# Performance work log

Measured on AMD Instinct MI355X. Metric: run time of the kernel, lower is better.

Reference implementation:

```python
import jax, jax.numpy as jnp
import numpy as np

N = 33554432  # number of flattened prediction/target points (~128 MB fp32 each)


def setup_inputs() -> dict:
    key = jax.random.key(0)
    k1, k2 = jax.random.split(key)
    predicted = jax.random.uniform(k1, (N,), dtype=jnp.float32)
    target = jax.random.uniform(k2, (N,), dtype=jnp.float32)
    weights = jnp.array([1.0, 2.0, 4.0, 8.0, 16.0], dtype=jnp.float32)
    edge = jnp.array([0.0, 0.1, 0.25, 0.5, 0.75, 1.0], dtype=jnp.float32)
    return {"predicted": predicted, "target": target, "weights": weights, "edge": edge}


def reference(predicted, target, weights, edge):
    # Original loops over bins: elements with edge[i] < t <= edge[i+1] get weight[i];
    # elements outside (edge[0], edge[-1]] are DROPPED (weight 0).
    nbins = weights.shape[0]
    # digitize(..., right=True): returns i s.t. edge[i-1] < t <= edge[i]; shift to bin index
    bin_idx = jnp.digitize(target, edge, right=True) - 1  # [N] int
    valid = (bin_idx >= 0) & (bin_idx < nbins)
    w = jnp.where(valid, weights[jnp.clip(bin_idx, 0, nbins - 1)], 0.0)
    loss = jnp.sum(w * (predicted - target) ** 2) / jnp.sum(weights)
    return loss
```

## Files before the change

### kernel.cpp

```cpp
#include <hip/hip_runtime.h>


#define NSLOTS 2048

__global__ void wmse_zero_ws(float* __restrict__ ws) {
    ws[blockIdx.x * blockDim.x + threadIdx.x] = 0.0f;
}

__device__ __forceinline__ float wmse_elem(float p, float t,
                                           float e0, float e1, float e2,
                                           float e3, float e4, float e5,
                                           float w0, float w1, float w2,
                                           float w3, float w4) {
    float w = 0.0f;
    w = (t > e0 && t <= e1) ? w0 : w;
    w = (t > e1 && t <= e2) ? w1 : w;
    w = (t > e2 && t <= e3) ? w2 : w;
    w = (t > e3 && t <= e4) ? w3 : w;
    w = (t > e4 && t <= e5) ? w4 : w;
    float d = p - t;
    return w * d * d;
}

__global__ __launch_bounds__(256) void WeightedMSELoss_60335700574782_kernel(
    const float* __restrict__ pred, const float* __restrict__ targ,
    const float* __restrict__ edge, const float* __restrict__ weights,
    float* __restrict__ partial, long long n4) {
    const float e0 = edge[0], e1 = edge[1], e2 = edge[2];
    const float e3 = edge[3], e4 = edge[4], e5 = edge[5];
    const float w0 = weights[0], w1 = weights[1], w2 = weights[2];
    const float w3 = weights[3], w4 = weights[4];

    const long long i = (long long)blockIdx.x * blockDim.x + threadIdx.x;
    const float4* __restrict__ p4 = (const float4*)pred;
    const float4* __restrict__ t4 = (const float4*)targ;

    float acc = 0.0f;
    if (i < n4) {
        float4 p = p4[i];
        float4 t = t4[i];
        acc  = wmse_elem(p.x, t.x, e0, e1, e2, e3, e4, e5, w0, w1, w2, w3, w4);
        acc += wmse_elem(p.y, t.y, e0, e1, e2, e3, e4, e5, w0, w1, w2, w3, w4);
        acc += wmse_elem(p.z, t.z, e0, e1, e2, e3, e4, e5, w0, w1, w2, w3, w4);
        acc += wmse_elem(p.w, t.w, e0, e1, e2, e3, e4, e5, w0, w1, w2, w3, w4);
    }

    #pragma unroll
    for (int off = 32; off > 0; off >>= 1)
        acc += __shfl_down(acc, off, 64);

    __shared__ float smem[4];
    const int lane = threadIdx.x & 63;
    const int wid = threadIdx.x >> 6;
    if (lane == 0) smem[wid] = acc;
    __syncthreads();
    if (threadIdx.x == 0) {
        float bsum = smem[0] + smem[1] + smem[2] + smem[3];
        atomicAdd(&partial[blockIdx.x & (NSLOTS - 1)], bsum);
    }
}

__global__ __launch_bounds__(256) void wmse_finish_kernel(
    const float* __restrict__ partial,
    const float* __restrict__ pred, const float* __restrict__ targ,
    const float* __restrict__ edge, const float* __restrict__ weights,
    float* __restrict__ out, long long n) {
    const float e0 = edge[0], e1 = edge[1], e2 = edge[2];
    const float e3 = edge[3], e4 = edge[4], e5 = edge[5];
    const float w0 = weights[0], w1 = weights[1], w2 = weights[2];
    const float w3 = weights[3], w4 = weights[4];
    const float inv_wsum = 1.0f / (w0 + w1 + w2 + w3 + w4);

    float acc = 0.0f;
    for (int i = threadIdx.x; i < NSLOTS; i += blockDim.x)
        acc += partial[i];

    const long long n4 = n >> 2;
    for (long long j = (n4 << 2) + threadIdx.x; j < n; j += blockDim.x)
        acc += wmse_elem(pred[j], targ[j], e0, e1, e2, e3, e4, e5, w0, w1, w2, w3, w4);

    #pragma unroll
    for (int off = 32; off > 0; off >>= 1)
        acc += __shfl_down(acc, off, 64);

    __shared__ float smem[4];
    const int lane = threadIdx.x & 63;
    const int wid = threadIdx.x >> 6;
    if (lane == 0) smem[wid] = acc;
    __syncthreads();
    if (threadIdx.x == 0)
        out[0] = (smem[0] + smem[1] + smem[2] + smem[3]) * inv_wsum;
}

extern "C" void kernel_launch(void* const* d_in, const int* in_sizes, int n_in,
                              void* d_out, int out_size, void* d_ws, size_t ws_size,
                              hipStream_t stream) {
    const float* pred    = (const float*)d_in[0];
    const float* targ    = (const float*)d_in[1];
    const float* weights = (const float*)d_in[2];
    const float* edge    = (const float*)d_in[3];
    float* out = (float*)d_out;
    float* partial = (float*)d_ws;
    const long long n = (long long)in_sizes[0];
    const long long n4 = n >> 2;

    wmse_zero_ws<<<NSLOTS / 256, 256, 0, stream>>>(partial);

    const int block = 256;
    const int grid = (int)((n4 + block - 1) / block);
    WeightedMSELoss_60335700574782_kernel<<<grid, block, 0, stream>>>(
        pred, targ, edge, weights, partial, n4);

    wmse_finish_kernel<<<1, block, 0, stream>>>(
        partial, pred, targ, edge, weights, out, n);
}
```

Measured before the change: 272.8 us.

## Process eight float4s per thread and write per-block partials without atomics

Each thread now loads eight float4 pairs up front and reduces them with four independent accumulators, so each block covers 2048 float4s and the grid is eight times smaller. Each block writes its sum to its own slot in the workspace, which removes the workspace-zeroing kernel and the atomic adds. The finish kernel now reduces a variable number of partials (4096 here) and handles the leftover tail. More loads in flight per thread give more memory-level parallelism, at the cost of higher register use and a serial finish loop that is twice as long.

```diff
diff --git a/kernel.cpp b/kernel.cpp
--- a/kernel.cpp
+++ b/kernel.cpp
@@ -1,11 +1,5 @@
 #include <hip/hip_runtime.h>
 
-
-#define NSLOTS 2048
-
-__global__ void wmse_zero_ws(float* __restrict__ ws) {
-    ws[blockIdx.x * blockDim.x + threadIdx.x] = 0.0f;
-}
 
 __device__ __forceinline__ float wmse_elem(float p, float t,
                                            float e0, float e1, float e2,
@@ -22,28 +16,49 @@
     return w * d * d;
 }
 
+#define WMSE4(p, t) (                                                          \
+    wmse_elem((p).x, (t).x, e0, e1, e2, e3, e4, e5, w0, w1, w2, w3, w4) +      \
+    wmse_elem((p).y, (t).y, e0, e1, e2, e3, e4, e5, w0, w1, w2, w3, w4) +      \
+    wmse_elem((p).z, (t).z, e0, e1, e2, e3, e4, e5, w0, w1, w2, w3, w4) +      \
+    wmse_elem((p).w, (t).w, e0, e1, e2, e3, e4, e5, w0, w1, w2, w3, w4))
+
+#define PER_BLOCK_F4 2048LL
+
 __global__ __launch_bounds__(256) void WeightedMSELoss_60335700574782_kernel(
     const float* __restrict__ pred, const float* __restrict__ targ,
     const float* __restrict__ edge, const float* __restrict__ weights,
-    float* __restrict__ partial, long long n4) {
+    float* __restrict__ partial) {
     const float e0 = edge[0], e1 = edge[1], e2 = edge[2];
     const float e3 = edge[3], e4 = edge[4], e5 = edge[5];
     const float w0 = weights[0], w1 = weights[1], w2 = weights[2];
     const float w3 = weights[3], w4 = weights[4];
 
-    const long long i = (long long)blockIdx.x * blockDim.x + threadIdx.x;
     const float4* __restrict__ p4 = (const float4*)pred;
     const float4* __restrict__ t4 = (const float4*)targ;
+    const long long base = (long long)blockIdx.x * PER_BLOCK_F4 + threadIdx.x;
 
-    float acc = 0.0f;
-    if (i < n4) {
-        float4 p = p4[i];
-        float4 t = t4[i];
-        acc  = wmse_elem(p.x, t.x, e0, e1, e2, e3, e4, e5, w0, w1, w2, w3, w4);
-        acc += wmse_elem(p.y, t.y, e0, e1, e2, e3, e4, e5, w0, w1, w2, w3, w4);
-        acc += wmse_elem(p.z, t.z, e0, e1, e2, e3, e4, e5, w0, w1, w2, w3, w4);
-        acc += wmse_elem(p.w, t.w, e0, e1, e2, e3, e4, e5, w0, w1, w2, w3, w4);
-    }
+    float4 pa = p4[base + 0 * 256];
+    float4 ta = t4[base + 0 * 256];
+    float4 pb = p4[base + 1 * 256];
+    float4 tb = t4[base + 1 * 256];
+    float4 pc = p4[base + 2 * 256];
+    float4 tc = t4[base + 2 * 256];
+    float4 pd = p4[base + 3 * 256];
+    float4 td = t4[base + 3 * 256];
+    float4 pe = p4[base + 4 * 256];
+    float4 te = t4[base + 4 * 256];
+    float4 pf = p4[base + 5 * 256];
+    float4 tf = t4[base + 5 * 256];
+    float4 pg = p4[base + 6 * 256];
+    float4 tg = t4[base + 6 * 256];
+    float4 ph = p4[base + 7 * 256];
+    float4 th = t4[base + 7 * 256];
+
+    float acc0 = WMSE4(pa, ta) + WMSE4(pe, te);
+    float acc1 = WMSE4(pb, tb) + WMSE4(pf, tf);
+    float acc2 = WMSE4(pc, tc) + WMSE4(pg, tg);
+    float acc3 = WMSE4(pd, td) + WMSE4(ph, th);
+    float acc = (acc0 + acc1) + (acc2 + acc3);
 
     #pragma unroll
     for (int off = 32; off > 0; off >>= 1)
@@ -54,17 +69,15 @@
     const int wid = threadIdx.x >> 6;
     if (lane == 0) smem[wid] = acc;
     __syncthreads();
-    if (threadIdx.x == 0) {
-        float bsum = smem[0] + smem[1] + smem[2] + smem[3];
-        atomicAdd(&partial[blockIdx.x & (NSLOTS - 1)], bsum);
-    }
+    if (threadIdx.x == 0)
+        partial[blockIdx.x] = smem[0] + smem[1] + smem[2] + smem[3];
 }
 
 __global__ __launch_bounds__(256) void wmse_finish_kernel(
-    const float* __restrict__ partial,
+    const float* __restrict__ partial, int nparts,
     const float* __restrict__ pred, const float* __restrict__ targ,
     const float* __restrict__ edge, const float* __restrict__ weights,
-    float* __restrict__ out, long long n) {
+    float* __restrict__ out, long long tail_start, long long n) {
     const float e0 = edge[0], e1 = edge[1], e2 = edge[2];
     const float e3 = edge[3], e4 = edge[4], e5 = edge[5];
     const float w0 = weights[0], w1 = weights[1], w2 = weights[2];
@@ -72,11 +85,10 @@
     const float inv_wsum = 1.0f / (w0 + w1 + w2 + w3 + w4);
 
     float acc = 0.0f;
-    for (int i = threadIdx.x; i < NSLOTS; i += blockDim.x)
+    for (int i = threadIdx.x; i < nparts; i += blockDim.x)
         acc += partial[i];
 
-    const long long n4 = n >> 2;
-    for (long long j = (n4 << 2) + threadIdx.x; j < n; j += blockDim.x)
+    for (long long j = tail_start + threadIdx.x; j < n; j += blockDim.x)
         acc += wmse_elem(pred[j], targ[j], e0, e1, e2, e3, e4, e5, w0, w1, w2, w3, w4);
 
     #pragma unroll
@@ -104,13 +116,13 @@
     const long long n = (long long)in_sizes[0];
     const long long n4 = n >> 2;
 
-    wmse_zero_ws<<<NSLOTS / 256, 256, 0, stream>>>(partial);
+    const int grid = (int)(n4 / PER_BLOCK_F4);
+    const long long tail_start = (long long)grid * PER_BLOCK_F4 * 4;
 
-    const int block = 256;
-    const int grid = (int)((n4 + block - 1) / block);
-    WeightedMSELoss_60335700574782_kernel<<<grid, block, 0, stream>>>(
-        pred, targ, edge, weights, partial, n4);
-
-    wmse_finish_kernel<<<1, block, 0, stream>>>(
-        partial, pred, targ, edge, weights, out, n);
+    if (grid > 0) {
+        WeightedMSELoss_60335700574782_kernel<<<grid, 256, 0, stream>>>(
+            pred, targ, edge, weights, partial);
+    }
+    wmse_finish_kernel<<<1, 256, 0, stream>>>(
+        partial, grid, pred, targ, edge, weights, out, tail_start, n);
 }
```

New measurement: 284.0 us. +4.1%, slower.
